# Performance work log

Measured on AMD Instinct MI355X. Metric: run time of the kernel, lower is better.

The kernel has to match this reference:

```python
import jax, jax.numpy as jnp
import numpy as np

RADIUS = 1.0
SIGMA = 0.16                 # w = relu(1 - d^2 / sigma), as in EPN's linear interpolation
N_NEIGHBOR = 32
KERNEL_CONDENSE_RATIO = 0.7


def ball_query(xyz, radius, n_neighbor):
    # xyz: [b,3,p]; stride==1 so query set == support set.
    pts = xyz.transpose(0, 2, 1)                      # [b,p,3]
    sq = jnp.sum(pts * pts, -1)                       # [b,p]
    d2 = sq[:, :, None] + sq[:, None, :] - 2.0 * jnp.einsum('bqd,bpd->bqp', pts, pts)
    p = pts.shape[1]
    # first n_neighbor points (in index order) within the ball; pad with first valid
    keys = jnp.where(d2 < radius * radius, jnp.arange(p)[None, None, :], p)   # [b,q,p] int
    vals, _ = jax.lax.top_k(-keys, n_neighbor)        # n_neighbor smallest keys
    cand = -vals                                      # candidate indices, ascending
    idx = jnp.where(cand < p, cand, cand[..., :1])    # self (d2=0) is always valid
    grouped = jax.vmap(lambda pt, i: pt[i])(pts, idx)  # [b,q,nn,3]
    rel = grouped - pts[:, :, None, :]                # local (relative) coordinates
    return idx, rel.transpose(0, 3, 1, 2)             # idx [b,q,nn], rel [b,3,q,nn]


def forward(xyz, feats, W, anchors, kernels):
    b, c_in, p, na = feats.shape
    ks = kernels.shape[0]
    idx, gxyz = ball_query(xyz, RADIUS, N_NEIGHBOR)   # [b,p,nn], [b,3,p,nn]
    # anchor-rotated kernel points: [na,ks,3]
    rk = jnp.einsum('aij,kj->aki', anchors, kernels)
    # squared distances neighbor <-> rotated kernel point, via |x|^2+|k|^2-2<x,k>
    dot = jnp.einsum('aki,bipn->bakpn', rk, gxyz)     # [b,na,ks,p,nn]
    d2 = (jnp.sum(gxyz * gxyz, 1)[:, None, None]
          + jnp.sum(rk * rk, -1)[None, :, :, None, None]
          - 2.0 * dot)
    inter_w = jax.nn.relu(1.0 - d2 / SIGMA)           # [b,na,ks,p,nn]
    # gather neighbor features: [b,c,p,nn,na]
    gf = jax.vmap(lambda f, i: f[:, i, :])(feats, idx)
    # kernel-weighted neighbor aggregation -> [b,c,ks,p,na]
    new_feats = jnp.einsum('bcpna,bakpn->bckpa', gf, inter_w)
    # BasicSO3Conv: W [dim_out, c_in*ks] @ [b, c_in*ks, p*na]
    dim_out = W.shape[0]
    out = jnp.einsum('oc,bcm->bom', W, new_feats.reshape(b, c_in * ks, p * na))
    return out.reshape(b, dim_out, p, na)


def setup_inputs() -> dict:
    key = jax.random.key(0)
    k1, k2, k3, k4, k5, k6 = jax.random.split(key, 6)
    b, p, c_in, c_out, na, ks = 1, 1024, 32, 64, 60, 24
    xyz = jax.random.normal(k1, (b, 3, p), dtype=jnp.float32)
    feats = jax.random.normal(k2, (b, c_in, p, na), dtype=jnp.float32)
    W = jax.random.normal(k3, (c_out, c_in * ks), dtype=jnp.float32) / np.float32(np.sqrt(c_in * ks))
    # proper rotation matrices (stand-in for the icosahedral anchors)
    A = jax.random.normal(k4, (na, 3, 3), dtype=jnp.float32)
    Q, _ = jnp.linalg.qr(A)
    anchors = Q * jnp.sign(jnp.linalg.det(Q))[:, None, None]
    # kernel points uniform in ball of radius 0.7*RADIUS (stand-in for the ply kernel)
    dirs = jax.random.normal(k5, (ks, 3), dtype=jnp.float32)
    dirs = dirs / jnp.linalg.norm(dirs, axis=-1, keepdims=True)
    r = (jax.random.uniform(k6, (ks, 1), dtype=jnp.float32) ** (1.0 / 3.0)) * (KERNEL_CONDENSE_RATIO * RADIUS)
    kernels = dirs * r
    return {"xyz": xyz, "feats": feats, "W": W, "anchors": anchors, "kernels": kernels}


def reference(xyz, feats, W, anchors, kernels):
    return forward(xyz, feats, W, anchors, kernels)
```

## Files before the change

### kernel.cpp

```cpp
#include <hip/hip_runtime.h>

typedef __attribute__((ext_vector_type(8))) short short8;
typedef __attribute__((ext_vector_type(4))) float f32x4;
typedef __attribute__((ext_vector_type(4))) unsigned int uint4v;

#define P_PTS   1024
#define NN      32
#define NA      60
#define KS      24
#define CIN     32
#define COUT    64
#define AC      12
#define NCH     5
#define SA      968
#define GF_SHORTS (AC*16*72)

union frag_u { uint4v u; short8 s; };

__device__ __forceinline__ unsigned short f2bf(float f) {
  unsigned int u = __float_as_uint(f);
  u += 0x7FFFu + ((u >> 16) & 1u);
  return (unsigned short)(u >> 16);
}
__device__ __forceinline__ unsigned int bfpair(float a, float b) {
  unsigned int ua = __float_as_uint(a) + 0x8000u;
  unsigned int ub = __float_as_uint(b) + 0x8000u;
  return __builtin_amdgcn_perm(ub, ua, 0x07060302u);
}
__device__ __forceinline__ void ilv(unsigned int u, unsigned int v,
                                    unsigned int& lo, unsigned int& hi) {
  lo = __builtin_amdgcn_perm(v, u, 0x05040100u);
  hi = __builtin_amdgcn_perm(v, u, 0x07060302u);
}

__device__ __forceinline__ float wcalc(const float4 rk, const float4 rl) {
  return fmaxf(0.0f, fmaf(rk.x, rl.x, fmaf(rk.y, rl.y, fmaf(rk.z, rl.z, rk.w + rl.w))));
}

#define SETUP_BLOCKS 1310

__global__ __launch_bounds__(256) void setup_kernel(
    const float* __restrict__ xyz, const float* __restrict__ feats,
    const float* __restrict__ Wm, const float* __restrict__ anchors,
    const float* __restrict__ kernels, int* __restrict__ ws_idx,
    unsigned short* __restrict__ ws_ft, unsigned short* __restrict__ ws_wbf,
    float4* __restrict__ ws_rk4)
{
  const int b   = blockIdx.x;
  const int tid = threadIdx.x;

  __shared__ float sx[P_PTS], sy[P_PTS], sz[P_PTS], sq[P_PTS];
  __shared__ int s_loc[4][NN];
  __shared__ unsigned short s_t[CIN*NA];

  if (b < 256) {
    for (int i = tid; i < P_PTS; i += 256) {
      float x = xyz[i], y = xyz[P_PTS + i], z = xyz[2*P_PTS + i];
      sx[i] = x; sy[i] = y; sz[i] = z;
      sq[i] = x*x + y*y + z*z;
    }
    __syncthreads();
    const int wave = tid >> 6, lane = tid & 63;
    const int q = b*4 + wave;
    const float xq = sx[q], yq = sy[q], zq = sz[q], sqq = sq[q];
    int cnt = 0;
    for (int jb = 0; jb < P_PTS; jb += 64) {
      const int j = jb + lane;
      const float d2 = sqq + sq[j] - 2.0f*(xq*sx[j] + yq*sy[j] + zq*sz[j]);
      const bool pred = d2 < 1.0f;
      const unsigned long long mask = __ballot(pred);
      if (pred) {
        const int slot = cnt + __popcll(mask & ((1ull << lane) - 1ull));
        if (slot < NN) s_loc[wave][slot] = j;
      }
      cnt += (int)__popcll(mask);
      if (cnt >= NN) break;
    }
    __syncthreads();
    const int cntc = cnt < NN ? cnt : NN;
    if (lane >= cntc && lane < NN) s_loc[wave][lane] = s_loc[wave][0];
    __syncthreads();
    if (lane < NN) ws_idx[q*NN + lane] = s_loc[wave][lane];
  } else if (b < 1280) {
    const int p = b - 256;
    for (int e = tid; e < CIN*NA; e += 256) {
      const int c = e / NA, a = e - c*NA;
      s_t[e] = f2bf(feats[c*(P_PTS*NA) + p*NA + a]);
    }
    __syncthreads();
    unsigned int* out32 = (unsigned int*)(ws_ft + p*(CIN*NA));
    for (int e = tid; e < (CIN*NA)/2; e += 256) {
      const int a = e >> 4, cu = e & 15;
      const unsigned int lo = s_t[(2*cu    )*NA + a];
      const unsigned int hi = s_t[(2*cu + 1)*NA + a];
      out32[a*16 + cu] = lo | (hi << 16);
    }
  } else if (b < 1304) {
    const int t = (b - 1280)*256 + tid;
    const int w = t / 1536;
    const int r = t - w*1536;
    const int s = r >> 6;
    const int lane = r & 63;
    const int quad = lane >> 4, lq = lane & 15;
    const int o = w*16 + lq;
    unsigned short h[8];
    #pragma unroll
    for (int j = 0; j < 8; ++j)
      h[j] = f2bf(Wm[o*(CIN*KS) + (quad*8 + j)*KS + s]);
    *(uint4*)(ws_wbf + (size_t)t*8) = *(const uint4*)h;
  } else {
    const int u = (b - 1304)*256 + tid;
    if (u < NA*KS) {
      const int a = u / KS, k = u - a*KS;
      const float rx = anchors[a*9+0]*kernels[k*3+0] + anchors[a*9+1]*kernels[k*3+1] + anchors[a*9+2]*kernels[k*3+2];
      const float ry = anchors[a*9+3]*kernels[k*3+0] + anchors[a*9+4]*kernels[k*3+1] + anchors[a*9+5]*kernels[k*3+2];
      const float rz = anchors[a*9+6]*kernels[k*3+0] + anchors[a*9+7]*kernels[k*3+1] + anchors[a*9+8]*kernels[k*3+2];
      ws_rk4[u] = make_float4(12.5f*rx, 12.5f*ry, 12.5f*rz,
                              1.0f - 6.25f*(rx*rx + ry*ry + rz*rz));
    }
  }
}

__global__ __launch_bounds__(256, 4) void conv_mfma(
    const float* __restrict__ xyz, const unsigned short* __restrict__ ft,
    const unsigned short* __restrict__ Wf, const int* __restrict__ g_idx,
    const float4* __restrict__ g_rk4, float* __restrict__ out)
{
  const int p    = blockIdx.x;
  const int tid  = threadIdx.x;
  const int wave = tid >> 6;
  const int lane = tid & 63;
  const int quad = lane >> 4;
  const int lq   = lane & 15;

  __shared__ __align__(16) unsigned short s_buf[GF_SHORTS];
  __shared__ __align__(16) float4 s_rel4[NN];
  __shared__ __align__(16) float4 s_rk4[AC*KS];

  if (tid < NN) {
    const int j = g_idx[p*NN + tid];
    const float rx = xyz[j]           - xyz[p];
    const float ry = xyz[P_PTS + j]   - xyz[P_PTS + p];
    const float rz = xyz[2*P_PTS + j] - xyz[2*P_PTS + p];
    s_rel4[tid] = make_float4(rx, ry, rz, -6.25f*(rx*rx + ry*ry + rz*rz));
  }
  const int np = (tid >> 2) & 15;
  const int ce = tid & 3;
  const int i0 = g_idx[p*NN + 2*np];
  const int i1 = g_idx[p*NN + 2*np + 1];
  const unsigned short* ft0 = ft + (size_t)i0*(CIN*NA) + ce*8;
  const unsigned short* ft1 = ft + (size_t)i1*(CIN*NA) + ce*8;

  uint4 pu[3], pv[3];
  #pragma unroll
  for (int i = 0; i < 3; ++i) {
    const int ag = i*4 + wave;
    pu[i] = *(const uint4*)(ft0 + ag*CIN);
    pv[i] = *(const uint4*)(ft1 + ag*CIN);
  }

  const unsigned int* bufd = (const unsigned int*)s_buf;
  const unsigned short* wptr = Wf + (size_t)wave*(24*512) + lane*8;

  for (int ch = 0; ch < NCH; ++ch) {
    const int a0 = ch * AC;

    for (int e = tid; e < AC*KS; e += 256) s_rk4[e] = g_rk4[a0*KS + e];
    #pragma unroll
    for (int i = 0; i < 3; ++i) {
      const int a = i*4 + wave;
      unsigned short* dst = &s_buf[a*1152 + np*72 + ce*16];
      uint4v w0, w1;
      unsigned int d0, d1;
      ilv(pu[i].x, pv[i].x, d0, d1); w0[0] = d0; w0[1] = d1;
      ilv(pu[i].y, pv[i].y, d0, d1); w0[2] = d0; w0[3] = d1;
      ilv(pu[i].z, pv[i].z, d0, d1); w1[0] = d0; w1[1] = d1;
      ilv(pu[i].w, pv[i].w, d0, d1); w1[2] = d0; w1[3] = d1;
      *(uint4v*)(dst)     = w0;
      *(uint4v*)(dst + 8) = w1;
    }
    __syncthreads();

    f32x4 acc1[3][2][2] = {};
    #pragma unroll
    for (int t = 0; t < 3; ++t) {
      const int a = wave*3 + t;
      const int based = a*576 + quad*144 + lq;
      frag_u af0, af1;
      #pragma unroll
      for (int i = 0; i < 4; ++i) {
        af0.u[i] = bufd[based + 36*i];
        af1.u[i] = bufd[based + 36*i + 16];
      }
      const int k1 = (lq < 8) ? (16 + lq) : 23;
      const float4 rk0 = s_rk4[a*KS + lq];
      const float4 rk1 = s_rk4[a*KS + k1];
      frag_u b0, b1;
      #pragma unroll
      for (int i = 0; i < 4; ++i) {
        const float4 rA = s_rel4[quad*8 + 2*i];
        const float4 rB = s_rel4[quad*8 + 2*i + 1];
        b0.u[i] = bfpair(wcalc(rk0, rA), wcalc(rk0, rB));
        b1.u[i] = bfpair(wcalc(rk1, rA), wcalc(rk1, rB));
      }
      acc1[t][0][0] = __builtin_amdgcn_mfma_f32_16x16x32_bf16(af0.s, b0.s, acc1[t][0][0], 0, 0, 0);
      acc1[t][0][1] = __builtin_amdgcn_mfma_f32_16x16x32_bf16(af0.s, b1.s, acc1[t][0][1], 0, 0, 0);
      acc1[t][1][0] = __builtin_amdgcn_mfma_f32_16x16x32_bf16(af1.s, b0.s, acc1[t][1][0], 0, 0, 0);
      acc1[t][1][1] = __builtin_amdgcn_mfma_f32_16x16x32_bf16(af1.s, b1.s, acc1[t][1][1], 0, 0, 0);
    }
    __syncthreads();

    #pragma unroll
    for (int t = 0; t < 3; ++t) {
      const int a = wave*3 + t;
      unsigned short* row = &s_buf[a*SA];
      uint2 pk;
      pk.x = bfpair(acc1[t][0][0][0], acc1[t][0][0][1]);
      pk.y = bfpair(acc1[t][0][0][2], acc1[t][0][0][3]);
      *(uint2*)&row[lq*40 + quad*4] = pk;
      pk.x = bfpair(acc1[t][1][0][0], acc1[t][1][0][1]);
      pk.y = bfpair(acc1[t][1][0][2], acc1[t][1][0][3]);
      *(uint2*)&row[lq*40 + 16 + quad*4] = pk;
      if (lq < 8) {
        pk.x = bfpair(acc1[t][0][1][0], acc1[t][0][1][1]);
        pk.y = bfpair(acc1[t][0][1][2], acc1[t][0][1][3]);
        *(uint2*)&row[(16+lq)*40 + quad*4] = pk;
        pk.x = bfpair(acc1[t][1][1][0], acc1[t][1][1][1]);
        pk.y = bfpair(acc1[t][1][1][2], acc1[t][1][1][3]);
        *(uint2*)&row[(16+lq)*40 + 16 + quad*4] = pk;
      }
    }
    __syncthreads();

    if (ch + 1 < NCH) {
      #pragma unroll
      for (int i = 0; i < 3; ++i) {
        const int ag = (ch + 1)*AC + i*4 + wave;
        pu[i] = *(const uint4*)(ft0 + ag*CIN);
        pv[i] = *(const uint4*)(ft1 + ag*CIN);
      }
    }

    const int acl = (lq < AC) ? lq : (AC - 1);
    const unsigned short* nptr = &s_buf[acl*SA + quad*8];
    f32x4 accA = {0.f,0.f,0.f,0.f}, accB = {0.f,0.f,0.f,0.f};
    #pragma unroll 4
    for (int s = 0; s < 24; s += 2) {
      const short8 aw0 = *(const short8*)(wptr + s*512);
      const short8 bn0 = *(const short8*)(nptr + s*40);
      const short8 aw1 = *(const short8*)(wptr + s*512 + 512);
      const short8 bn1 = *(const short8*)(nptr + s*40 + 40);
      accA = __builtin_amdgcn_mfma_f32_16x16x32_bf16(aw0, bn0, accA, 0, 0, 0);
      accB = __builtin_amdgcn_mfma_f32_16x16x32_bf16(aw1, bn1, accB, 0, 0, 0);
    }

    if (lq < AC) {
      const int ob = wave*16 + quad*4;
      #pragma unroll
      for (int r = 0; r < 4; ++r)
        out[(size_t)(ob + r)*(P_PTS*NA) + p*NA + a0 + lq] = accA[r] + accB[r];
    }
    __syncthreads();
  }
}

extern "C" void kernel_launch(void* const* d_in, const int* in_sizes, int n_in,
                              void* d_out, int out_size, void* d_ws, size_t ws_size,
                              hipStream_t stream) {
  const float* xyz     = (const float*)d_in[0];
  const float* feats   = (const float*)d_in[1];
  const float* Wm      = (const float*)d_in[2];
  const float* anchors = (const float*)d_in[3];
  const float* kernels = (const float*)d_in[4];
  float* out = (float*)d_out;

  unsigned short* ws_wbf = (unsigned short*)d_ws;
  int*    ws_idx = (int*)((char*)d_ws + 98304);
  float4* ws_rk4 = (float4*)((char*)d_ws + 98304 + 131072);
  unsigned short* ws_ft = (unsigned short*)((char*)d_ws + 98304 + 131072 + 23040);

  hipLaunchKernelGGL(setup_kernel, dim3(SETUP_BLOCKS), dim3(256), 0, stream,
                     xyz, feats, Wm, anchors, kernels, ws_idx, ws_ft, ws_wbf, ws_rk4);
  hipLaunchKernelGGL(conv_mfma, dim3(P_PTS), dim3(256), 0, stream,
                     xyz, ws_ft, ws_wbf, ws_idx, ws_rk4, out);
}
```

Baseline: 111.6 us.

## Process anchors in chunks of 16 to fill MFMA lanes in the W-GEMM

Replaces the five 12-anchor chunks with three 16-anchor chunks plus one 12-anchor chunk, using a templated chunk body. The second-stage MFMA then uses all 16 columns for most chunks instead of wasting 4 of them, and the number of chunk iterations and barriers drops from five to four. Rotated kernel points are now read straight from global memory rather than staged through shared memory. The larger shared buffer (16 anchors' worth) and the extra per-thread prefetch registers could reduce occupancy.

Result: faster. 107.0 us (-4.1%).

```diff
diff --git a/kernel.cpp b/kernel.cpp
--- a/kernel.cpp
+++ b/kernel.cpp
@@ -10,10 +10,8 @@
 #define KS      24
 #define CIN     32
 #define COUT    64
-#define AC      12
-#define NCH     5
 #define SA      968
-#define GF_SHORTS (AC*16*72)
+#define GF_SHORTS (16*1152)
 
 union frag_u { uint4v u; short8 s; };
 
@@ -121,6 +119,113 @@
   }
 }
 
+template<int NAW, int NAWN>
+__device__ __forceinline__ void chunk_body(
+    const int a0, const int wave, const int quad, const int lq,
+    const int np, const int ce,
+    const unsigned short* __restrict__ ft0, const unsigned short* __restrict__ ft1,
+    unsigned short* __restrict__ s_buf, const float4* __restrict__ s_rel4,
+    const float4* __restrict__ g_rk4, const unsigned short* __restrict__ wptr,
+    float* __restrict__ out, const int p, uint4* pu, uint4* pv)
+{
+  constexpr int NACH = NAW * 4;
+
+  #pragma unroll
+  for (int i = 0; i < NAW; ++i) {
+    const int a = i*4 + wave;
+    unsigned short* dst = &s_buf[a*1152 + np*72 + ce*16];
+    uint4v w0, w1;
+    unsigned int d0, d1;
+    ilv(pu[i].x, pv[i].x, d0, d1); w0[0] = d0; w0[1] = d1;
+    ilv(pu[i].y, pv[i].y, d0, d1); w0[2] = d0; w0[3] = d1;
+    ilv(pu[i].z, pv[i].z, d0, d1); w1[0] = d0; w1[1] = d1;
+    ilv(pu[i].w, pv[i].w, d0, d1); w1[2] = d0; w1[3] = d1;
+    *(uint4v*)(dst)     = w0;
+    *(uint4v*)(dst + 8) = w1;
+  }
+  __syncthreads();
+
+  const unsigned int* bufd = (const unsigned int*)s_buf;
+  f32x4 acc1[NAW][2][2] = {};
+  #pragma unroll
+  for (int t = 0; t < NAW; ++t) {
+    const int a = wave*NAW + t;
+    const int based = a*576 + quad*144 + lq;
+    frag_u af0, af1;
+    #pragma unroll
+    for (int i = 0; i < 4; ++i) {
+      af0.u[i] = bufd[based + 36*i];
+      af1.u[i] = bufd[based + 36*i + 16];
+    }
+    const int k1 = (lq < 8) ? (16 + lq) : 23;
+    const float4 rk0 = g_rk4[(a0 + a)*KS + lq];
+    const float4 rk1 = g_rk4[(a0 + a)*KS + k1];
+    frag_u b0, b1;
+    #pragma unroll
+    for (int i = 0; i < 4; ++i) {
+      const float4 rA = s_rel4[quad*8 + 2*i];
+      const float4 rB = s_rel4[quad*8 + 2*i + 1];
+      b0.u[i] = bfpair(wcalc(rk0, rA), wcalc(rk0, rB));
+      b1.u[i] = bfpair(wcalc(rk1, rA), wcalc(rk1, rB));
+    }
+    acc1[t][0][0] = __builtin_amdgcn_mfma_f32_16x16x32_bf16(af0.s, b0.s, acc1[t][0][0], 0, 0, 0);
+    acc1[t][0][1] = __builtin_amdgcn_mfma_f32_16x16x32_bf16(af0.s, b1.s, acc1[t][0][1], 0, 0, 0);
+    acc1[t][1][0] = __builtin_amdgcn_mfma_f32_16x16x32_bf16(af1.s, b0.s, acc1[t][1][0], 0, 0, 0);
+    acc1[t][1][1] = __builtin_amdgcn_mfma_f32_16x16x32_bf16(af1.s, b1.s, acc1[t][1][1], 0, 0, 0);
+  }
+  __syncthreads();
+
+  #pragma unroll
+  for (int t = 0; t < NAW; ++t) {
+    const int a = wave*NAW + t;
+    unsigned short* row = &s_buf[a*SA];
+    uint2 pk;
+    pk.x = bfpair(acc1[t][0][0][0], acc1[t][0][0][1]);
+    pk.y = bfpair(acc1[t][0][0][2], acc1[t][0][0][3]);
+    *(uint2*)&row[lq*40 + quad*4] = pk;
+    pk.x = bfpair(acc1[t][1][0][0], acc1[t][1][0][1]);
+    pk.y = bfpair(acc1[t][1][0][2], acc1[t][1][0][3]);
+    *(uint2*)&row[lq*40 + 16 + quad*4] = pk;
+    if (lq < 8) {
+      pk.x = bfpair(acc1[t][0][1][0], acc1[t][0][1][1]);
+      pk.y = bfpair(acc1[t][0][1][2], acc1[t][0][1][3]);
+      *(uint2*)&row[(16+lq)*40 + quad*4] = pk;
+      pk.x = bfpair(acc1[t][1][1][0], acc1[t][1][1][1]);
+      pk.y = bfpair(acc1[t][1][1][2], acc1[t][1][1][3]);
+      *(uint2*)&row[(16+lq)*40 + 16 + quad*4] = pk;
+    }
+  }
+  __syncthreads();
+
+  #pragma unroll
+  for (int i = 0; i < NAWN; ++i) {
+    const int ag = a0 + NACH + i*4 + wave;
+    pu[i] = *(const uint4*)(ft0 + ag*CIN);
+    pv[i] = *(const uint4*)(ft1 + ag*CIN);
+  }
+
+  const int acl = (NACH >= 16) ? lq : ((lq < NACH) ? lq : (NACH - 1));
+  const unsigned short* nptr = &s_buf[acl*SA + quad*8];
+  f32x4 accA = {0.f,0.f,0.f,0.f}, accB = {0.f,0.f,0.f,0.f};
+  #pragma unroll 4
+  for (int s = 0; s < 24; s += 2) {
+    const short8 aw0 = *(const short8*)(wptr + s*512);
+    const short8 bn0 = *(const short8*)(nptr + s*40);
+    const short8 aw1 = *(const short8*)(wptr + s*512 + 512);
+    const short8 bn1 = *(const short8*)(nptr + s*40 + 40);
+    accA = __builtin_amdgcn_mfma_f32_16x16x32_bf16(aw0, bn0, accA, 0, 0, 0);
+    accB = __builtin_amdgcn_mfma_f32_16x16x32_bf16(aw1, bn1, accB, 0, 0, 0);
+  }
+
+  if (NACH >= 16 || lq < NACH) {
+    const int ob = wave*16 + quad*4;
+    #pragma unroll
+    for (int r = 0; r < 4; ++r)
+      out[(size_t)(ob + r)*(P_PTS*NA) + p*NA + a0 + lq] = accA[r] + accB[r];
+  }
+  __syncthreads();
+}
+
 __global__ __launch_bounds__(256, 4) void conv_mfma(
     const float* __restrict__ xyz, const unsigned short* __restrict__ ft,
     const unsigned short* __restrict__ Wf, const int* __restrict__ g_idx,
@@ -135,7 +240,6 @@
 
   __shared__ __align__(16) unsigned short s_buf[GF_SHORTS];
   __shared__ __align__(16) float4 s_rel4[NN];
-  __shared__ __align__(16) float4 s_rk4[AC*KS];
 
   if (tid < NN) {
     const int j = g_idx[p*NN + tid];
@@ -151,117 +255,19 @@
   const unsigned short* ft0 = ft + (size_t)i0*(CIN*NA) + ce*8;
   const unsigned short* ft1 = ft + (size_t)i1*(CIN*NA) + ce*8;
 
-  uint4 pu[3], pv[3];
-  #pragma unroll
-  for (int i = 0; i < 3; ++i) {
+  uint4 pu[4], pv[4];
+  #pragma unroll
+  for (int i = 0; i < 4; ++i) {
     const int ag = i*4 + wave;
     pu[i] = *(const uint4*)(ft0 + ag*CIN);
     pv[i] = *(const uint4*)(ft1 + ag*CIN);
   }
-
-  const unsigned int* bufd = (const unsigned int*)s_buf;
   const unsigned short* wptr = Wf + (size_t)wave*(24*512) + lane*8;
 
-  for (int ch = 0; ch < NCH; ++ch) {
-    const int a0 = ch * AC;
-
-    for (int e = tid; e < AC*KS; e += 256) s_rk4[e] = g_rk4[a0*KS + e];
-    #pragma unroll
-    for (int i = 0; i < 3; ++i) {
-      const int a = i*4 + wave;
-      unsigned short* dst = &s_buf[a*1152 + np*72 + ce*16];
-      uint4v w0, w1;
-      unsigned int d0, d1;
-      ilv(pu[i].x, pv[i].x, d0, d1); w0[0] = d0; w0[1] = d1;
-      ilv(pu[i].y, pv[i].y, d0, d1); w0[2] = d0; w0[3] = d1;
-      ilv(pu[i].z, pv[i].z, d0, d1); w1[0] = d0; w1[1] = d1;
-      ilv(pu[i].w, pv[i].w, d0, d1); w1[2] = d0; w1[3] = d1;
-      *(uint4v*)(dst)     = w0;
-      *(uint4v*)(dst + 8) = w1;
-    }
-    __syncthreads();
-
-    f32x4 acc1[3][2][2] = {};
-    #pragma unroll
-    for (int t = 0; t < 3; ++t) {
-      const int a = wave*3 + t;
-      const int based = a*576 + quad*144 + lq;
-      frag_u af0, af1;
-      #pragma unroll
-      for (int i = 0; i < 4; ++i) {
-        af0.u[i] = bufd[based + 36*i];
-        af1.u[i] = bufd[based + 36*i + 16];
-      }
-      const int k1 = (lq < 8) ? (16 + lq) : 23;
-      const float4 rk0 = s_rk4[a*KS + lq];
-      const float4 rk1 = s_rk4[a*KS + k1];
-      frag_u b0, b1;
-      #pragma unroll
-      for (int i = 0; i < 4; ++i) {
-        const float4 rA = s_rel4[quad*8 + 2*i];
-        const float4 rB = s_rel4[quad*8 + 2*i + 1];
-        b0.u[i] = bfpair(wcalc(rk0, rA), wcalc(rk0, rB));
-        b1.u[i] = bfpair(wcalc(rk1, rA), wcalc(rk1, rB));
-      }
-      acc1[t][0][0] = __builtin_amdgcn_mfma_f32_16x16x32_bf16(af0.s, b0.s, acc1[t][0][0], 0, 0, 0);
-      acc1[t][0][1] = __builtin_amdgcn_mfma_f32_16x16x32_bf16(af0.s, b1.s, acc1[t][0][1], 0, 0, 0);
-      acc1[t][1][0] = __builtin_amdgcn_mfma_f32_16x16x32_bf16(af1.s, b0.s, acc1[t][1][0], 0, 0, 0);
-      acc1[t][1][1] = __builtin_amdgcn_mfma_f32_16x16x32_bf16(af1.s, b1.s, acc1[t][1][1], 0, 0, 0);
-    }
-    __syncthreads();
-
-    #pragma unroll
-    for (int t = 0; t < 3; ++t) {
-      const int a = wave*3 + t;
-      unsigned short* row = &s_buf[a*SA];
-      uint2 pk;
-      pk.x = bfpair(acc1[t][0][0][0], acc1[t][0][0][1]);
-      pk.y = bfpair(acc1[t][0][0][2], acc1[t][0][0][3]);
-      *(uint2*)&row[lq*40 + quad*4] = pk;
-      pk.x = bfpair(acc1[t][1][0][0], acc1[t][1][0][1]);
-      pk.y = bfpair(acc1[t][1][0][2], acc1[t][1][0][3]);
-      *(uint2*)&row[lq*40 + 16 + quad*4] = pk;
-      if (lq < 8) {
-        pk.x = bfpair(acc1[t][0][1][0], acc1[t][0][1][1]);
-        pk.y = bfpair(acc1[t][0][1][2], acc1[t][0][1][3]);
-        *(uint2*)&row[(16+lq)*40 + quad*4] = pk;
-        pk.x = bfpair(acc1[t][1][1][0], acc1[t][1][1][1]);
-        pk.y = bfpair(acc1[t][1][1][2], acc1[t][1][1][3]);
-        *(uint2*)&row[(16+lq)*40 + 16 + quad*4] = pk;
-      }
-    }
-    __syncthreads();
-
-    if (ch + 1 < NCH) {
-      #pragma unroll
-      for (int i = 0; i < 3; ++i) {
-        const int ag = (ch + 1)*AC + i*4 + wave;
-        pu[i] = *(const uint4*)(ft0 + ag*CIN);
-        pv[i] = *(const uint4*)(ft1 + ag*CIN);
-      }
-    }
-
-    const int acl = (lq < AC) ? lq : (AC - 1);
-    const unsigned short* nptr = &s_buf[acl*SA + quad*8];
-    f32x4 accA = {0.f,0.f,0.f,0.f}, accB = {0.f,0.f,0.f,0.f};
-    #pragma unroll 4
-    for (int s = 0; s < 24; s += 2) {
-      const short8 aw0 = *(const short8*)(wptr + s*512);
-      const short8 bn0 = *(const short8*)(nptr + s*40);
-      const short8 aw1 = *(const short8*)(wptr + s*512 + 512);
-      const short8 bn1 = *(const short8*)(nptr + s*40 + 40);
-      accA = __builtin_amdgcn_mfma_f32_16x16x32_bf16(aw0, bn0, accA, 0, 0, 0);
-      accB = __builtin_amdgcn_mfma_f32_16x16x32_bf16(aw1, bn1, accB, 0, 0, 0);
-    }
-
-    if (lq < AC) {
-      const int ob = wave*16 + quad*4;
-      #pragma unroll
-      for (int r = 0; r < 4; ++r)
-        out[(size_t)(ob + r)*(P_PTS*NA) + p*NA + a0 + lq] = accA[r] + accB[r];
-    }
-    __syncthreads();
-  }
+  chunk_body<4,4>( 0, wave, quad, lq, np, ce, ft0, ft1, s_buf, s_rel4, g_rk4, wptr, out, p, pu, pv);
+  chunk_body<4,4>(16, wave, quad, lq, np, ce, ft0, ft1, s_buf, s_rel4, g_rk4, wptr, out, p, pu, pv);
+  chunk_body<4,3>(32, wave, quad, lq, np, ce, ft0, ft1, s_buf, s_rel4, g_rk4, wptr, out, p, pu, pv);
+  chunk_body<3,0>(48, wave, quad, lq, np, ce, ft0, ft1, s_buf, s_rel4, g_rk4, wptr, out, p, pu, pv);
 }
 
 extern "C" void kernel_launch(void* const* d_in, const int* in_sizes, int n_in,
```
